# Kernel tuning notes

Measured on AMD Instinct MI355X. Metric: run time of the kernel, lower is better.

Reference implementation:

```python
import jax, jax.numpy as jnp
import numpy as np
import math

B, S, D_MODEL, H, D_K = 8, 1024, 512, 8, 64


def setup_inputs() -> dict:
    key = jax.random.key(0)
    ks = jax.random.split(key, 12)
    s = 1.0 / math.sqrt(D_MODEL)
    inp = {
        "q": jax.random.normal(ks[0], (B, S, D_MODEL), dtype=jnp.float32),
        "k": jax.random.normal(ks[1], (B, S, D_MODEL), dtype=jnp.float32),
        "v": jax.random.normal(ks[2], (B, S, D_MODEL), dtype=jnp.float32),
        "Wq": jax.random.normal(ks[3], (D_MODEL, D_MODEL), dtype=jnp.float32) * s,
        "bq": jnp.zeros((D_MODEL,), dtype=jnp.float32),
        "Wk": jax.random.normal(ks[4], (D_MODEL, D_MODEL), dtype=jnp.float32) * s,
        "bk": jnp.zeros((D_MODEL,), dtype=jnp.float32),
        "Wv": jax.random.normal(ks[5], (D_MODEL, D_MODEL), dtype=jnp.float32) * s,
        "bv": jnp.zeros((D_MODEL,), dtype=jnp.float32),
        "Wo": jax.random.normal(ks[6], (D_MODEL, D_MODEL), dtype=jnp.float32) * s,
        "bo": jnp.zeros((D_MODEL,), dtype=jnp.float32),
        # xavier_uniform on (H,1,1): bound = sqrt(6/(1+1)) ~ 1.732
        "gammas": jax.random.uniform(ks[7], (H, 1, 1), minval=-1.732, maxval=1.732, dtype=jnp.float32),
        "mask": jnp.triu(jnp.ones((S, S), dtype=bool), k=1),  # mask future positions
        "key_padding_mask": jnp.zeros((B, S), dtype=bool),
    }
    return inp


def reference(q, k, v, Wq, bq, Wk, bk, Wv, bv, Wo, bo, gammas, mask, key_padding_mask):
    bs, seqlen = q.shape[0], q.shape[1]
    NEG = -1e32

    def proj(x, W, b):
        # nn.Linear: x @ W.T + b, then split heads -> [b, h, s, d_k]
        return (x @ W.T + b).reshape(bs, seqlen, H, D_K).transpose(0, 2, 1, 3)

    qh, kh, vh = proj(q, Wq, bq), proj(k, Wk, bk), proj(v, Wv, bv)

    scores = jnp.einsum("bhqd,bhkd->bhqk", qh, kh) / math.sqrt(D_K)
    full_mask = mask[None, None, :, :] | key_padding_mask[:, None, None, :]  # [b,1,s,s] bcast over h

    # --- distance-decay branch (torch.no_grad / detach) ---
    scores_ = jax.nn.softmax(jnp.where(full_mask, NEG, scores), axis=-1)
    scores_ = scores_ * (~full_mask).astype(scores.dtype)
    distcum = jnp.cumsum(scores_, axis=-1)  # forward=True
    disttotal = jnp.sum(scores_, axis=-1, keepdims=True)
    idx = jnp.arange(seqlen)
    position_effect = jnp.abs(idx[None, :] - idx[:, None]).astype(scores.dtype)  # |i-j|
    dist_scores = jnp.sqrt(jnp.clip((disttotal - distcum) * position_effect, 0.0))
    dist_scores = jax.lax.stop_gradient(dist_scores)

    gamma = -jax.nn.softplus(gammas)[None]  # [1, h, 1, 1]
    total_effect = jnp.clip(jnp.exp(dist_scores * gamma), 1e-5, 1e5)

    attn = jax.nn.softmax(jnp.where(full_mask, NEG, scores * total_effect), axis=-1)
    out = jnp.einsum("bhqk,bhkd->bhqd", attn, vh)
    concat = out.transpose(0, 2, 1, 3).reshape(bs, seqlen, D_MODEL)
    return concat @ Wo.T + bo
```

## Files before the change

### kernel.cpp

```cpp
#include <hip/hip_runtime.h>
#include <hip/hip_bf16.h>
#include <math.h>

#define NB   8
#define NS   1024
#define NDM  512
#define NH   8
#define NDK  64
#define NM   8192

typedef __attribute__((ext_vector_type(8))) short short8;
typedef __attribute__((ext_vector_type(4))) float f32x4;

__device__ __forceinline__ unsigned short f2b(float f) {
    __hip_bfloat16 h = __float2bfloat16(f);
    unsigned short u;
    __builtin_memcpy(&u, &h, 2);
    return u;
}
__device__ __forceinline__ float b2f(unsigned short u) {
    return __uint_as_float(((unsigned)u) << 16);
}
__device__ __forceinline__ float exp2_raw(float x) { float r; asm("v_exp_f32 %0, %1" : "=v"(r) : "v"(x)); return r; }
__device__ __forceinline__ float sqrt_raw(float x) { float r; asm("v_sqrt_f32 %0, %1" : "=v"(r) : "v"(x)); return r; }
__device__ __forceinline__ float rcp_raw(float x)  { float r; asm("v_rcp_f32 %0, %1" : "=v"(r) : "v"(x)); return r; }

__device__ __forceinline__ short8 pack8(float4 a, float4 b) {
    short8 r;
    r[0] = (short)f2b(a.x); r[1] = (short)f2b(a.y);
    r[2] = (short)f2b(a.z); r[3] = (short)f2b(a.w);
    r[4] = (short)f2b(b.x); r[5] = (short)f2b(b.y);
    r[6] = (short)f2b(b.z); r[7] = (short)f2b(b.w);
    return r;
}

template<int OMODE, bool ACVT>
__device__ __forceinline__ void gemm_body(unsigned short* As, unsigned short* Bs,
                                          const void* __restrict__ Ap,
                                          const float* __restrict__ Wf,
                                          const float* __restrict__ bias,
                                          void* __restrict__ outp) {
    const int tid  = threadIdx.x;
    const int lane = tid & 63;
    const int wid  = tid >> 6;
    const int l15  = lane & 15, lhi = lane >> 4;
    const int m0 = (blockIdx.x >> 2) * 128;
    const int n0 = (blockIdx.x & 3) * 128;
    const int wr = wid >> 1, wc = wid & 1;

    const float* Af = (const float*)Ap;
    const unsigned short* Ab = (const unsigned short*)Ap;

    f32x4 acc[4][4];
#pragma unroll
    for (int i = 0; i < 4; ++i)
#pragma unroll
        for (int j = 0; j < 4; ++j) acc[i][j] = (f32x4){0.f, 0.f, 0.f, 0.f};

    for (int kk0 = 0; kk0 < NDM; kk0 += 32) {
#pragma unroll
        for (int c = 0; c < 2; ++c) {
            int ci  = tid + 256 * c;
            int row = ci >> 2;
            int kc  = (ci & 3) << 3;
            short8 aval;
            if (ACVT) {
                const float* p = Af + (size_t)(m0 + row) * NDM + kk0 + kc;
                aval = pack8(*(const float4*)p, *(const float4*)(p + 4));
            } else {
                aval = *(const short8*)(Ab + (size_t)(m0 + row) * NDM + kk0 + kc);
            }
            *(short8*)(As + ci * 8) = aval;
            const float* qp = Wf + (size_t)(n0 + row) * NDM + kk0 + kc;
            *(short8*)(Bs + ci * 8) = pack8(*(const float4*)qp, *(const float4*)(qp + 4));
        }
        __syncthreads();
        short8 af[4], bf[4];
#pragma unroll
        for (int mi = 0; mi < 4; ++mi)
            af[mi] = *(const short8*)(As + (wr * 64 + mi * 16 + l15) * 32 + lhi * 8);
#pragma unroll
        for (int ni = 0; ni < 4; ++ni)
            bf[ni] = *(const short8*)(Bs + (wc * 64 + ni * 16 + l15) * 32 + lhi * 8);
#pragma unroll
        for (int mi = 0; mi < 4; ++mi)
#pragma unroll
            for (int ni = 0; ni < 4; ++ni)
                acc[mi][ni] = __builtin_amdgcn_mfma_f32_16x16x32_bf16(af[mi], bf[ni], acc[mi][ni], 0, 0, 0);
        __syncthreads();
    }

#pragma unroll
    for (int mi = 0; mi < 4; ++mi) {
#pragma unroll
        for (int ni = 0; ni < 4; ++ni) {
            int row0 = m0 + wr * 64 + mi * 16 + lhi * 4;
            int col  = n0 + wc * 64 + ni * 16 + l15;
            float bv = bias[col];
            if (OMODE == 0) {
                unsigned short* o = (unsigned short*)outp;
                int h = col >> 6, d = col & 63;
#pragma unroll
                for (int r = 0; r < 4; ++r) {
                    int m = row0 + r;
                    int b = m >> 10, s = m & 1023;
                    o[(size_t)(((b * NH + h) * NS) + s) * NDK + d] = f2b(acc[mi][ni][r] + bv);
                }
            } else if (OMODE == 1) {
                unsigned short* o = (unsigned short*)outp;
                int h = col >> 6, d = col & 63;
                int b = row0 >> 10, s0 = row0 & 1023;
                ushort4 u;
                u.x = f2b(acc[mi][ni][0] + bv);
                u.y = f2b(acc[mi][ni][1] + bv);
                u.z = f2b(acc[mi][ni][2] + bv);
                u.w = f2b(acc[mi][ni][3] + bv);
                *(ushort4*)(o + (size_t)((b * NH + h) * NDK + d) * NS + s0) = u;
            } else {
                float* o = (float*)outp;
#pragma unroll
                for (int r = 0; r < 4; ++r)
                    o[(size_t)(row0 + r) * NDM + col] = acc[mi][ni][r] + bv;
            }
        }
    }
}

__global__ __launch_bounds__(256) void qkv_gemm(const float* __restrict__ q,
                                                const float* __restrict__ k,
                                                const float* __restrict__ v,
                                                const float* __restrict__ Wq,
                                                const float* __restrict__ Wk,
                                                const float* __restrict__ Wv,
                                                const float* __restrict__ bq,
                                                const float* __restrict__ bk,
                                                const float* __restrict__ bv,
                                                unsigned short* __restrict__ Qh,
                                                unsigned short* __restrict__ Kh,
                                                unsigned short* __restrict__ Vt) {
    __shared__ unsigned short As[128 * 32];
    __shared__ unsigned short Bs[128 * 32];
    const int y = blockIdx.y;
    if (y == 0)      gemm_body<0, true>(As, Bs, q, Wq, bq, Qh);
    else if (y == 1) gemm_body<0, true>(As, Bs, k, Wk, bk, Kh);
    else             gemm_body<1, true>(As, Bs, v, Wv, bv, Vt);
}

__global__ __launch_bounds__(256) void wo_gemm(const unsigned short* __restrict__ A,
                                               const float* __restrict__ Wo,
                                               const float* __restrict__ bo,
                                               float* __restrict__ out) {
    __shared__ unsigned short As[128 * 32];
    __shared__ unsigned short Bs[128 * 32];
    gemm_body<2, false>(As, Bs, A, Wo, bo, out);
}

__global__ __launch_bounds__(256, 4) void attn_kernel(const unsigned short* __restrict__ Qh,
                                                      const unsigned short* __restrict__ Kh,
                                                      const unsigned short* __restrict__ Vt,
                                                      const float* __restrict__ gammas,
                                                      unsigned short* __restrict__ concat) {
    __shared__ unsigned short pb[16 * 1024];
    __shared__ float l2s[16];
    const int bh   = blockIdx.x & 63;
    const int pair = blockIdx.x >> 6;
    const int tid = threadIdx.x, lane = tid & 63, wid = tid >> 6;
    const int l15 = lane & 15, lhi = lane >> 4;
    const float SC = 0.125f * 1.44269504f;

    const unsigned short* Kb = Kh + (size_t)bh * NS * NDK;
    const unsigned short* Vb = Vt + (size_t)bh * NDK * NS;
    const float g  = gammas[bh & (NH - 1)];
    const float g2 = -log1pf(__expf(g)) * 1.44269504f;
    const int cb = lane * 16;
    const int bq_ = bh >> 3, hq = bh & 7;

    for (int hs = 0; hs < 2; ++hs) {
        const int qt = hs ? (63 - pair) : pair;
        const int r0 = qt * 16;
        const int C  = ((r0 + 16 + 63) >> 6) << 6;

        const unsigned short* Qb = Qh + (size_t)(bh * NS + r0) * NDK;
        short8 qf0 = *(const short8*)(Qb + l15 * NDK + lhi * 8);
        short8 qf1 = *(const short8*)(Qb + l15 * NDK + lhi * 8 + 32);
        for (int j0 = wid * 16; j0 < C; j0 += 64) {
            const unsigned short* kp = Kb + (size_t)(j0 + l15) * NDK + lhi * 8;
            short8 kf0 = *(const short8*)kp;
            short8 kf1 = *(const short8*)(kp + 32);
            f32x4 a = {0.f, 0.f, 0.f, 0.f};
            a = __builtin_amdgcn_mfma_f32_16x16x32_bf16(kf0, qf0, a, 0, 0, 0);
            a = __builtin_amdgcn_mfma_f32_16x16x32_bf16(kf1, qf1, a, 0, 0, 0);
            ushort4 u;
            u.x = f2b(a[0] * SC);
            u.y = f2b(a[1] * SC);
            u.z = f2b(a[2] * SC);
            u.w = f2b(a[3] * SC);
            int ch = ((j0 >> 3) + (lhi >> 1)) ^ l15;
            *(ushort4*)(pb + l15 * 1024 + ch * 8 + (lhi & 1) * 4) = u;
        }
        __syncthreads();

#pragma unroll
        for (int t = 0; t < 4; ++t) {
            const int rr = wid + 4 * t;
            const int i  = r0 + rr;
            unsigned short* rowp = pb + rr * 1024;
            short8 raw0 = *(const short8*)(rowp + (((2 * lane)     ^ rr) << 3));
            short8 raw1 = *(const short8*)(rowp + (((2 * lane + 1) ^ rr) << 3));
            float s[16];
#pragma unroll
            for (int u = 0; u < 8; ++u) {
                s[u]     = b2f((unsigned short)raw0[u]);
                s[8 + u] = b2f((unsigned short)raw1[u]);
            }
#pragma unroll
            for (int u = 0; u < 16; ++u)
                if (cb + u > i) s[u] = -1e30f;
            float p[16];
            float run = 0.f;
#pragma unroll
            for (int u = 0; u < 16; ++u) { run += exp2_raw(s[u]); p[u] = run; }
            float inc = run;
#pragma unroll
            for (int off = 1; off < 64; off <<= 1) {
                float y = __shfl_up(inc, off);
                if (lane >= off) inc += y;
            }
            const float l1       = __shfl(inc, 63);
            const float invl1    = rcp_raw(l1);
            const float taillane = l1 - (inc - run);
            const float di       = (float)(i - cb);
            float l2 = 0.f;
            short8 h0, h1;
#pragma unroll
            for (int u = 0; u < 16; ++u) {
                float tail = fmaxf(taillane - p[u], 0.f);
                float t2   = (tail * invl1) * (di - (float)u);
                float te   = fmaxf(exp2_raw(g2 * sqrt_raw(t2)), 1e-5f);
                float w    = exp2_raw(s[u] * te);
                l2 += w;
                if (u < 8) h0[u] = (short)f2b(w); else h1[u - 8] = (short)f2b(w);
            }
#pragma unroll
            for (int off = 32; off; off >>= 1) l2 += __shfl_xor(l2, off);
            if (lane == 0) l2s[rr] = l2;
            *(short8*)(rowp + (((2 * lane)     ^ rr) << 3)) = h0;
            *(short8*)(rowp + (((2 * lane + 1) ^ rr) << 3)) = h1;
        }
        __syncthreads();

        const int d0 = wid * 16;
        f32x4 acc = {0.f, 0.f, 0.f, 0.f};
        for (int j0 = 0; j0 < C; j0 += 32) {
            short8 av = *(const short8*)(Vb + (size_t)(d0 + l15) * NS + j0 + lhi * 8);
            short8 pw = *(const short8*)(pb + l15 * 1024 + (((((j0 >> 3) + lhi)) ^ l15) << 3));
            acc = __builtin_amdgcn_mfma_f32_16x16x32_bf16(av, pw, acc, 0, 0, 0);
        }
        {
            float inv2 = rcp_raw(l2s[l15]);
            int d = d0 + lhi * 4;
            int s = r0 + l15;
            ushort4 u;
            u.x = f2b(acc[0] * inv2); u.y = f2b(acc[1] * inv2);
            u.z = f2b(acc[2] * inv2); u.w = f2b(acc[3] * inv2);
            *(ushort4*)(concat + (size_t)(bq_ * NS + s) * NDM + hq * NDK + d) = u;
        }
        __syncthreads();
    }
}

extern "C" void kernel_launch(void* const* d_in, const int* in_sizes, int n_in,
                              void* d_out, int out_size, void* d_ws, size_t ws_size,
                              hipStream_t stream) {
    const float* q  = (const float*)d_in[0];
    const float* k  = (const float*)d_in[1];
    const float* v  = (const float*)d_in[2];
    const float* Wq = (const float*)d_in[3];
    const float* bq = (const float*)d_in[4];
    const float* Wk = (const float*)d_in[5];
    const float* bk = (const float*)d_in[6];
    const float* Wv = (const float*)d_in[7];
    const float* bv = (const float*)d_in[8];
    const float* Wo = (const float*)d_in[9];
    const float* bo = (const float*)d_in[10];
    const float* gm = (const float*)d_in[11];

    char* w = (char*)d_ws;
    unsigned short* Qh     = (unsigned short*)(w);
    unsigned short* Kh     = (unsigned short*)(w + (size_t)8388608);
    unsigned short* Vt     = (unsigned short*)(w + (size_t)16777216);
    unsigned short* concat = (unsigned short*)(w + (size_t)25165824);

    qkv_gemm<<<dim3(256, 3), dim3(256), 0, stream>>>(q, k, v, Wq, Wk, Wv, bq, bk, bv, Qh, Kh, Vt);
    attn_kernel<<<dim3(2048), dim3(256), 0, stream>>>(Qh, Kh, Vt, gm, concat);
    wo_gemm<<<dim3(256), dim3(256), 0, stream>>>(concat, Wo, bo, (float*)d_out);
}
```

Measured before the change: 136.5 us.

## Pre-convert QKV weights, use direct global-to-LDS loads, trim causal softmax columns

A new kernel converts Wq/Wk/Wv to bf16 once into scratch space inside the output buffer. The QKV GEMM then loads those weights, and the Wo GEMM loads its bf16 activations, straight into LDS with global_load_lds, instead of converting or staging them through registers. In the attention row pass, each lane now handles only as many columns as the causal extent C needs (W per lane) rather than a fixed 16. This cuts exp, sqrt and LDS work for early query tiles. The cost is one extra kernel launch and reuse of d_out as temporary storage before wo_gemm overwrites it.

```diff
diff --git a/kernel.cpp b/kernel.cpp
--- a/kernel.cpp
+++ b/kernel.cpp
@@ -17,9 +17,6 @@
     unsigned short u;
     __builtin_memcpy(&u, &h, 2);
     return u;
-}
-__device__ __forceinline__ float b2f(unsigned short u) {
-    return __uint_as_float(((unsigned)u) << 16);
 }
 __device__ __forceinline__ float exp2_raw(float x) { float r; asm("v_exp_f32 %0, %1" : "=v"(r) : "v"(x)); return r; }
 __device__ __forceinline__ float sqrt_raw(float x) { float r; asm("v_sqrt_f32 %0, %1" : "=v"(r) : "v"(x)); return r; }
@@ -34,10 +31,29 @@
     return r;
 }
 
-template<int OMODE, bool ACVT>
+__device__ __forceinline__ void gload16(const unsigned short* g, unsigned short* l) {
+    __builtin_amdgcn_global_load_lds(
+        (const __attribute__((address_space(1))) void*)g,
+        (__attribute__((address_space(3))) void*)l, 16, 0, 0);
+}
+
+__global__ __launch_bounds__(256) void cvt_w3(const float* __restrict__ Wq,
+                                              const float* __restrict__ Wk,
+                                              const float* __restrict__ Wv,
+                                              unsigned short* __restrict__ out) {
+    int idx = blockIdx.x * 256 + threadIdx.x;
+    int m = idx >> 16;
+    const float* s = (m == 0) ? Wq : ((m == 1) ? Wk : Wv);
+    float4 f = *(const float4*)(s + (size_t)(idx & 65535) * 4);
+    ushort4 u;
+    u.x = f2b(f.x); u.y = f2b(f.y); u.z = f2b(f.z); u.w = f2b(f.w);
+    *(ushort4*)(out + (size_t)idx * 4) = u;
+}
+
+template<int OMODE, bool ACVT, bool BCVT>
 __device__ __forceinline__ void gemm_body(unsigned short* As, unsigned short* Bs,
                                           const void* __restrict__ Ap,
-                                          const float* __restrict__ Wf,
+                                          const void* __restrict__ Wp,
                                           const float* __restrict__ bias,
                                           void* __restrict__ outp) {
     const int tid  = threadIdx.x;
@@ -50,6 +66,8 @@
 
     const float* Af = (const float*)Ap;
     const unsigned short* Ab = (const unsigned short*)Ap;
+    const float* Wf = (const float*)Wp;
+    const unsigned short* Wb = (const unsigned short*)Wp;
 
     f32x4 acc[4][4];
 #pragma unroll
@@ -63,16 +81,18 @@
             int ci  = tid + 256 * c;
             int row = ci >> 2;
             int kc  = (ci & 3) << 3;
-            short8 aval;
             if (ACVT) {
                 const float* p = Af + (size_t)(m0 + row) * NDM + kk0 + kc;
-                aval = pack8(*(const float4*)p, *(const float4*)(p + 4));
+                *(short8*)(As + ci * 8) = pack8(*(const float4*)p, *(const float4*)(p + 4));
             } else {
-                aval = *(const short8*)(Ab + (size_t)(m0 + row) * NDM + kk0 + kc);
-            }
-            *(short8*)(As + ci * 8) = aval;
-            const float* qp = Wf + (size_t)(n0 + row) * NDM + kk0 + kc;
-            *(short8*)(Bs + ci * 8) = pack8(*(const float4*)qp, *(const float4*)(qp + 4));
+                gload16(Ab + (size_t)(m0 + row) * NDM + kk0 + kc, As + ci * 8);
+            }
+            if (BCVT) {
+                const float* qp = Wf + (size_t)(n0 + row) * NDM + kk0 + kc;
+                *(short8*)(Bs + ci * 8) = pack8(*(const float4*)qp, *(const float4*)(qp + 4));
+            } else {
+                gload16(Wb + (size_t)(n0 + row) * NDM + kk0 + kc, Bs + ci * 8);
+            }
         }
         __syncthreads();
         short8 af[4], bf[4];
@@ -129,9 +149,9 @@
 __global__ __launch_bounds__(256) void qkv_gemm(const float* __restrict__ q,
                                                 const float* __restrict__ k,
                                                 const float* __restrict__ v,
-                                                const float* __restrict__ Wq,
-                                                const float* __restrict__ Wk,
-                                                const float* __restrict__ Wv,
+                                                const unsigned short* __restrict__ Wqb,
+                                                const unsigned short* __restrict__ Wkb,
+                                                const unsigned short* __restrict__ Wvb,
                                                 const float* __restrict__ bq,
                                                 const float* __restrict__ bk,
                                                 const float* __restrict__ bv,
@@ -141,9 +161,9 @@
     __shared__ unsigned short As[128 * 32];
     __shared__ unsigned short Bs[128 * 32];
     const int y = blockIdx.y;
-    if (y == 0)      gemm_body<0, true>(As, Bs, q, Wq, bq, Qh);
-    else if (y == 1) gemm_body<0, true>(As, Bs, k, Wk, bk, Kh);
-    else             gemm_body<1, true>(As, Bs, v, Wv, bv, Vt);
+    if (y == 0)      gemm_body<0, true, false>(As, Bs, q, Wqb, bq, Qh);
+    else if (y == 1) gemm_body<0, true, false>(As, Bs, k, Wkb, bk, Kh);
+    else             gemm_body<1, true, false>(As, Bs, v, Wvb, bv, Vt);
 }
 
 __global__ __launch_bounds__(256) void wo_gemm(const unsigned short* __restrict__ A,
@@ -152,7 +172,7 @@
                                                float* __restrict__ out) {
     __shared__ unsigned short As[128 * 32];
     __shared__ unsigned short Bs[128 * 32];
-    gemm_body<2, false>(As, Bs, A, Wo, bo, out);
+    gemm_body<2, false, true>(As, Bs, A, Wo, bo, out);
 }
 
 __global__ __launch_bounds__(256, 4) void attn_kernel(const unsigned short* __restrict__ Qh,
@@ -172,13 +192,13 @@
     const unsigned short* Vb = Vt + (size_t)bh * NDK * NS;
     const float g  = gammas[bh & (NH - 1)];
     const float g2 = -log1pf(__expf(g)) * 1.44269504f;
-    const int cb = lane * 16;
     const int bq_ = bh >> 3, hq = bh & 7;
 
     for (int hs = 0; hs < 2; ++hs) {
         const int qt = hs ? (63 - pair) : pair;
         const int r0 = qt * 16;
         const int C  = ((r0 + 16 + 63) >> 6) << 6;
+        const int W  = ((C >> 6) + 1) & ~1;
 
         const unsigned short* Qb = Qh + (size_t)(bh * NS + r0) * NDK;
         short8 qf0 = *(const short8*)(Qb + l15 * NDK + lhi * 8);
@@ -205,21 +225,26 @@
             const int rr = wid + 4 * t;
             const int i  = r0 + rr;
             unsigned short* rowp = pb + rr * 1024;
-            short8 raw0 = *(const short8*)(rowp + (((2 * lane)     ^ rr) << 3));
-            short8 raw1 = *(const short8*)(rowp + (((2 * lane + 1) ^ rr) << 3));
-            float s[16];
-#pragma unroll
-            for (int u = 0; u < 8; ++u) {
-                s[u]     = b2f((unsigned short)raw0[u]);
-                s[8 + u] = b2f((unsigned short)raw1[u]);
-            }
+            const int cb = lane * W;
+            float s[16], p[16];
+            int idxs[8];
+#pragma unroll
+            for (int j = 0; j < 8; ++j) {
+                if (2 * j < W) {
+                    int c = cb + 2 * j;
+                    int idx = (((c >> 3) ^ rr) << 3) + (c & 7);
+                    idxs[j] = idx;
+                    unsigned int raw = *(const unsigned int*)(rowp + idx);
+                    float lo = __uint_as_float(raw << 16);
+                    float hi = __uint_as_float(raw & 0xffff0000u);
+                    s[2 * j]     = (c > i)     ? -1e30f : lo;
+                    s[2 * j + 1] = (c + 1 > i) ? -1e30f : hi;
+                }
+            }
+            float run = 0.f;
 #pragma unroll
             for (int u = 0; u < 16; ++u)
-                if (cb + u > i) s[u] = -1e30f;
-            float p[16];
-            float run = 0.f;
-#pragma unroll
-            for (int u = 0; u < 16; ++u) { run += exp2_raw(s[u]); p[u] = run; }
+                if (u < W) { run += exp2_raw(s[u]); p[u] = run; }
             float inc = run;
 #pragma unroll
             for (int off = 1; off < 64; off <<= 1) {
@@ -231,21 +256,32 @@
             const float taillane = l1 - (inc - run);
             const float di       = (float)(i - cb);
             float l2 = 0.f;
-            short8 h0, h1;
-#pragma unroll
-            for (int u = 0; u < 16; ++u) {
-                float tail = fmaxf(taillane - p[u], 0.f);
-                float t2   = (tail * invl1) * (di - (float)u);
-                float te   = fmaxf(exp2_raw(g2 * sqrt_raw(t2)), 1e-5f);
-                float w    = exp2_raw(s[u] * te);
-                l2 += w;
-                if (u < 8) h0[u] = (short)f2b(w); else h1[u - 8] = (short)f2b(w);
+#pragma unroll
+            for (int j = 0; j < 8; ++j) {
+                if (2 * j < W) {
+                    float w0, w1;
+                    {
+                        const int u = 2 * j;
+                        float tail = fmaxf(taillane - p[u], 0.f);
+                        float t2   = (tail * invl1) * (di - (float)u);
+                        float te   = fmaxf(exp2_raw(g2 * sqrt_raw(t2)), 1e-5f);
+                        w0 = exp2_raw(s[u] * te);
+                    }
+                    {
+                        const int u = 2 * j + 1;
+                        float tail = fmaxf(taillane - p[u], 0.f);
+                        float t2   = (tail * invl1) * (di - (float)u);
+                        float te   = fmaxf(exp2_raw(g2 * sqrt_raw(t2)), 1e-5f);
+                        w1 = exp2_raw(s[u] * te);
+                    }
+                    l2 += w0 + w1;
+                    unsigned int pkd = ((unsigned)f2b(w1) << 16) | (unsigned)f2b(w0);
+                    *(unsigned int*)(rowp + idxs[j]) = pkd;
+                }
             }
 #pragma unroll
             for (int off = 32; off; off >>= 1) l2 += __shfl_xor(l2, off);
             if (lane == 0) l2s[rr] = l2;
-            *(short8*)(rowp + (((2 * lane)     ^ rr) << 3)) = h0;
-            *(short8*)(rowp + (((2 * lane + 1) ^ rr) << 3)) = h1;
         }
         __syncthreads();
 
@@ -291,7 +327,12 @@
     unsigned short* Vt     = (unsigned short*)(w + (size_t)16777216);
     unsigned short* concat = (unsigned short*)(w + (size_t)25165824);
 
-    qkv_gemm<<<dim3(256, 3), dim3(256), 0, stream>>>(q, k, v, Wq, Wk, Wv, bq, bk, bv, Qh, Kh, Vt);
+    unsigned short* Wqb = (unsigned short*)d_out;
+    unsigned short* Wkb = Wqb + 262144;
+    unsigned short* Wvb = Wqb + 524288;
+
+    cvt_w3<<<dim3(768), dim3(256), 0, stream>>>(Wq, Wk, Wv, Wqb);
+    qkv_gemm<<<dim3(256, 3), dim3(256), 0, stream>>>(q, k, v, Wqb, Wkb, Wvb, bq, bk, bv, Qh, Kh, Vt);
     attn_kernel<<<dim3(2048), dim3(256), 0, stream>>>(Qh, Kh, Vt, gm, concat);
     wo_gemm<<<dim3(256), dim3(256), 0, stream>>>(concat, Wo, bo, (float*)d_out);
 }
```

Measured after the change: 141.8 us. 3.9% more time.
